# Performance work log

Measured on AMD Instinct MI355X. Metric: run time of the kernel, lower is better.

The kernel has to match this reference:

```python
import jax, jax.numpy as jnp
import numpy as np

B, C, T, H, W = 8, 512, 8, 28, 28
DI, DO = 256, 512  # dim_inner, dim_out
INIT_STD = 0.01
BN_EPS = 1e-5


def conv1x1(x, w, b):
    # 1x1x1 Conv3d == channel contraction. x: [B,C,T,H,W], w: [O,C], b: [O]
    return jnp.einsum('bcthw,oc->bothw', x, w) + b[None, :, None, None, None]


def setup_inputs() -> dict:
    key = jax.random.key(0)
    ks = jax.random.split(key, 8)
    x = jax.random.normal(ks[0], (B, C, T, H, W), jnp.float32)
    theta_w = INIT_STD * jax.random.normal(ks[1], (DI, C), jnp.float32)
    phi_w = INIT_STD * jax.random.normal(ks[2], (DI, C), jnp.float32)
    g_w = INIT_STD * jax.random.normal(ks[3], (DI, C), jnp.float32)
    out_w = INIT_STD * jax.random.normal(ks[4], (DO, DI), jnp.float32)
    theta_b = jnp.zeros((DI,), jnp.float32)
    phi_b = jnp.zeros((DI,), jnp.float32)
    g_b = jnp.zeros((DI,), jnp.float32)
    out_b = jnp.zeros((DO,), jnp.float32)
    bn_gamma = jnp.ones((DO,), jnp.float32)  # BN_INIT_GAMMA = 1.0
    bn_beta = jnp.zeros((DO,), jnp.float32)
    return {"x": x, "theta_w": theta_w, "theta_b": theta_b, "phi_w": phi_w,
            "phi_b": phi_b, "g_w": g_w, "g_b": g_b, "out_w": out_w,
            "out_b": out_b, "bn_gamma": bn_gamma, "bn_beta": bn_beta}


def reference(x, theta_w, theta_b, phi_w, phi_b, g_w, g_b, out_w, out_b, bn_gamma, bn_beta):
    b, c, t, h, w = x.shape
    scale = DI ** (-0.5)
    # theta on full resolution
    theta = conv1x1(x, theta_w, theta_b).reshape(b, DI, -1)          # [B,DI,N]
    # MaxPool3d((1,2,2)) with stride (1,2,2): H,W even -> block max
    mp = x.reshape(b, c, t, h // 2, 2, w // 2, 2).max(axis=(4, 6))   # [B,C,T,H/2,W/2]
    phi = conv1x1(mp, phi_w, phi_b).reshape(b, DI, -1)               # [B,DI,M]
    g = conv1x1(mp, g_w, g_b).reshape(b, DI, -1)                     # [B,DI,M]
    # attention: theta^T phi -> [B,N,M], scaled softmax over M
    logits = jnp.einsum('bdn,bdm->bnm', theta, phi) * scale
    p = jax.nn.softmax(logits, axis=-1)
    # t = g @ p^T -> [B,DI,N]
    tt = jnp.einsum('bdm,bnm->bdn', g, p).reshape(b, DI, t, h, w)
    out = conv1x1(tt, out_w, out_b)                                  # [B,DO,T,H,W]
    # BatchNorm3d (training-mode batch statistics over B,T,H,W)
    mean = out.mean(axis=(0, 2, 3, 4), keepdims=True)
    var = out.var(axis=(0, 2, 3, 4), keepdims=True)
    out = (out - mean) * jax.lax.rsqrt(var + BN_EPS)
    out = out * bn_gamma[None, :, None, None, None] + bn_beta[None, :, None, None, None]
    return out + x
```

## Files before the change

### kernel.cpp

```cpp
#include <hip/hip_runtime.h>
#include <hip/hip_bf16.h>

#define B_ 8
#define C_ 512
#define T_ 8
#define H_ 28
#define W_ 28
#define N_ (T_*H_*W_)
#define HP_ 14
#define WP_ 14
#define M_ (T_*HP_*WP_)
#define DI_ 256
#define DO_ 512
#define BN_EPS 1e-5f
#define SCALE_LOG2E 0.090168440055560214f
#define PSUM_COLS 392

typedef __attribute__((ext_vector_type(8))) short short8;
typedef __attribute__((ext_vector_type(4))) float float4v;
typedef __attribute__((ext_vector_type(2))) float float2v;

__device__ inline unsigned short f2bf(float f) {
    union { float f; unsigned int u; } v; v.f = f;
    unsigned int u = v.u;
    return (unsigned short)((u + 0x7FFFu + ((u >> 16) & 1u)) >> 16);
}
__device__ inline float bf2f(unsigned short h) {
    union { unsigned int u; float f; } v; v.u = ((unsigned int)h) << 16;
    return v.f;
}

__global__ void xpose_x(const float* __restrict__ x, unsigned short* __restrict__ xT) {
    __shared__ float tile[64][65];
    int b = blockIdx.z;
    int c0 = blockIdx.y * 64, n0 = blockIdx.x * 64;
    const float* src = x + (size_t)b * C_ * N_;
    int tx = threadIdx.x & 63, ty = threadIdx.x >> 6;
#pragma unroll
    for (int i = 0; i < 16; i++) {
        int c = ty + i * 4;
        tile[c][tx] = src[(size_t)(c0 + c) * N_ + n0 + tx];
    }
    __syncthreads();
    unsigned short* d = xT + ((size_t)b * N_ + n0) * C_ + c0;
#pragma unroll
    for (int i = 0; i < 16; i++) {
        int n = ty + i * 4;
        d[(size_t)n * C_ + tx] = f2bf(tile[tx][n]);
    }
}

__global__ void pool_xpose(const float* __restrict__ x, unsigned short* __restrict__ mpT) {
    __shared__ unsigned short tile[196][72];
    int b = blockIdx.z, t = blockIdx.y, c0 = blockIdx.x * 64;
    const float* src = x + (((size_t)b * C_ + c0) * T_ + t) * 784;
    for (int idx = threadIdx.x; idx < 64 * 196; idx += 256) {
        int cc = idx / 196, p = idx - cc * 196;
        int hp = p / 14, wp = p - hp * 14;
        const float* r0 = src + (size_t)cc * T_ * 784 + (2 * hp) * 28 + 2 * wp;
        float2v a = *(const float2v*)r0;
        float2v c = *(const float2v*)(r0 + 28);
        float m = fmaxf(fmaxf(a.x, a.y), fmaxf(c.x, c.y));
        tile[p][cc] = f2bf(m);
    }
    __syncthreads();
    unsigned short* d = mpT + ((size_t)b * M_ + t * 196) * C_ + c0;
    for (int idx = threadIdx.x; idx < 196 * 64; idx += 256) {
        int p = idx >> 6, cc = idx & 63;
        d[(size_t)p * C_ + cc] = tile[p][cc];
    }
}

__global__ void cast_w(const float* __restrict__ s, unsigned short* __restrict__ d, int n) {
    int i = blockIdx.x * 256 + threadIdx.x;
    if (i < n) d[i] = f2bf(s[i]);
}

template<int BIAS_MODE>
__global__ __launch_bounds__(256) void btgemm(
        const unsigned short* __restrict__ A, size_t strideAb,
        const unsigned short* __restrict__ Bm, size_t strideBb,
        unsigned short* __restrict__ Dp, size_t strideDb,
        const float* __restrict__ bias, int Mdim, int Ndim, int Kdim) {
    int b = blockIdx.z;
    const unsigned short* Ab = A + (size_t)b * strideAb;
    const unsigned short* Bb = Bm + (size_t)b * strideBb;
    int m0 = blockIdx.x * 64, n0 = blockIdx.y * 64;
    int wave = threadIdx.x >> 6, lane = threadIdx.x & 63;
    int wm = (wave >> 1) * 32, wn = (wave & 1) * 32;
    int lr = lane & 15, lk = lane >> 4;
    float4v acc[2][2] = {};
    for (int k0 = 0; k0 < Kdim; k0 += 32) {
        short8 a[2], bb[2];
#pragma unroll
        for (int i = 0; i < 2; i++) {
            int ar = m0 + wm + i * 16 + lr; if (ar >= Mdim) ar = Mdim - 1;
            a[i] = *(const short8*)(Ab + (size_t)ar * Kdim + k0 + lk * 8);
            int br = n0 + wn + i * 16 + lr; if (br >= Ndim) br = Ndim - 1;
            bb[i] = *(const short8*)(Bb + (size_t)br * Kdim + k0 + lk * 8);
        }
#pragma unroll
        for (int i = 0; i < 2; i++)
#pragma unroll
            for (int j = 0; j < 2; j++)
                acc[i][j] = __builtin_amdgcn_mfma_f32_16x16x32_bf16(a[i], bb[j], acc[i][j], 0, 0, 0);
    }
#pragma unroll
    for (int i = 0; i < 2; i++)
#pragma unroll
        for (int j = 0; j < 2; j++) {
            int col = n0 + wn + j * 16 + lr;
#pragma unroll
            for (int r = 0; r < 4; r++) {
                int row = m0 + wm + i * 16 + lk * 4 + r;
                if (row < Mdim && col < Ndim) {
                    float v = acc[i][j][r];
                    if (BIAS_MODE == 1) v += bias[col];
                    else if (BIAS_MODE == 2) v += bias[row];
                    Dp[(size_t)b * strideDb + (size_t)row * Ndim + col] = f2bf(v);
                }
            }
        }
}

__global__ __launch_bounds__(256, 2) void theta_gemm(
        const unsigned short* __restrict__ xT, const unsigned short* __restrict__ wq,
        unsigned short* __restrict__ thetaT, const float* __restrict__ bias) {
    __shared__ __align__(16) unsigned short wqs[2][32][512];
    const int bid = blockIdx.x;
    const int b = bid & 7;
    const int nblk = bid >> 3;
    const int wave = threadIdx.x >> 6, lane = threadIdx.x & 63;
    const int lr = lane & 15, lk = lane >> 4;
    const unsigned short* Ab = xT + ((size_t)b * N_ + nblk * 128 + wave * 32) * C_;

    short8 a[2][16];
#pragma unroll
    for (int i = 0; i < 2; i++)
#pragma unroll
        for (int kd = 0; kd < 16; kd++)
            a[i][kd] = *(const short8*)(Ab + (size_t)(i * 16 + lr) * C_ + kd * 32 + lk * 8);

    auto stage = [&](int bufi, int t) {
#pragma unroll
        for (int j = 0; j < 8; j++) {
            int row = wave * 8 + j;
            int qq = (lane * 16) ^ ((row & 7) << 4);
            const unsigned short* src = wq + (size_t)(t * 32 + row) * C_ + (qq >> 1);
            unsigned short* dst = &wqs[bufi][0][0] + row * 512;
            __builtin_amdgcn_global_load_lds(
                (const __attribute__((address_space(1))) unsigned int*)src,
                (__attribute__((address_space(3))) unsigned int*)dst, 16, 0, 0);
        }
    };

    stage(0, 0);
    const int hq = (lk * 16) ^ ((lr & 7) << 4);
    unsigned short* D = thetaT + ((size_t)b * N_ + nblk * 128 + wave * 32) * DI_;
    int buf = 0;
#pragma unroll
    for (int t = 0; t < 8; t++) {
        if (t < 7) {
            stage(buf ^ 1, t + 1);
            asm volatile("s_waitcnt vmcnt(8)" ::: "memory");
        } else {
            asm volatile("s_waitcnt vmcnt(0)" ::: "memory");
        }
        __syncthreads();
        const char* W = (const char*)&wqs[buf][0][0];
        float4v acc[2][2] = {};
#pragma unroll
        for (int kd = 0; kd < 16; kd++) {
            short8 b0 = *(const short8*)(W + lr * 1024 + ((kd * 64) ^ hq));
            short8 b1 = *(const short8*)(W + (16 + lr) * 1024 + ((kd * 64) ^ hq));
            acc[0][0] = __builtin_amdgcn_mfma_f32_16x16x32_bf16(a[0][kd], b0, acc[0][0], 0, 0, 0);
            acc[0][1] = __builtin_amdgcn_mfma_f32_16x16x32_bf16(a[0][kd], b1, acc[0][1], 0, 0, 0);
            acc[1][0] = __builtin_amdgcn_mfma_f32_16x16x32_bf16(a[1][kd], b0, acc[1][0], 0, 0, 0);
            acc[1][1] = __builtin_amdgcn_mfma_f32_16x16x32_bf16(a[1][kd], b1, acc[1][1], 0, 0, 0);
        }
#pragma unroll
        for (int i = 0; i < 2; i++)
#pragma unroll
            for (int j = 0; j < 2; j++) {
                int col = t * 32 + j * 16 + lr;
                float bv = bias[col];
#pragma unroll
                for (int r = 0; r < 4; r++) {
                    int row = i * 16 + lk * 4 + r;
                    D[(size_t)row * DI_ + col] = f2bf(acc[i][j][r] + bv);
                }
            }
        __syncthreads();
        buf ^= 1;
    }
}

__global__ __launch_bounds__(256, 2) void out_gemm(
        const unsigned short* __restrict__ wo,
        const unsigned short* __restrict__ Bh, const unsigned short* __restrict__ Bl,
        float* __restrict__ Dp, const float* __restrict__ bias,
        float* __restrict__ psum) {
    __shared__ __align__(16) unsigned short tts[2][2][32][256];
    const int bid = blockIdx.x;
    const int b = bid & 7;
    const int rem = bid >> 3;
    const int doblk = rem & 3;
    const int nchunk = rem >> 2;
    const int wave = threadIdx.x >> 6, lane = threadIdx.x & 63;
    const int lr = lane & 15, lk = lane >> 4;
    const unsigned short* Ab = wo + (size_t)(doblk * 128 + wave * 32) * DI_;
    const unsigned short* BhB = Bh + ((size_t)b * N_ + nchunk * 128) * DI_;
    const unsigned short* BlB = Bl + ((size_t)b * N_ + nchunk * 128) * DI_;

    short8 a[2][8];
#pragma unroll
    for (int i = 0; i < 2; i++)
#pragma unroll
        for (int kd = 0; kd < 8; kd++)
            a[i][kd] = *(const short8*)(Ab + (size_t)(i * 16 + lr) * DI_ + kd * 32 + lk * 8);

    auto stage = [&](int bufi, int t) {
#pragma unroll
        for (int p = 0; p < 2; p++) {
            const unsigned short* S = p ? BlB : BhB;
#pragma unroll
            for (int j = 0; j < 4; j++) {
                int chunk = wave * 4 + j;
                int row = chunk * 2 + (lane >> 5);
                int qq = (((lane & 31) * 16)) ^ ((row & 7) << 4);
                const unsigned short* src = S + (size_t)(t * 32 + row) * DI_ + (qq >> 1);
                unsigned short* dst = &tts[bufi][p][0][0] + chunk * 512;
                __builtin_amdgcn_global_load_lds(
                    (const __attribute__((address_space(1))) unsigned int*)src,
                    (__attribute__((address_space(3))) unsigned int*)dst, 16, 0, 0);
            }
        }
    };

    stage(0, 0);
    const int hq = (lk * 16) ^ ((lr & 7) << 4);
    float4v acc[4][2][2] = {};
    int buf = 0;
#pragma unroll
    for (int t = 0; t < 4; t++) {
        if (t < 3) {
            stage(buf ^ 1, t + 1);
            asm volatile("s_waitcnt vmcnt(8)" ::: "memory");
        } else {
            asm volatile("s_waitcnt vmcnt(0)" ::: "memory");
        }
        __syncthreads();
        const char* th = (const char*)&tts[buf][0][0][0];
        const char* tl = (const char*)&tts[buf][1][0][0];
#pragma unroll
        for (int kd = 0; kd < 8; kd++) {
            short8 bh0 = *(const short8*)(th + lr * 512 + ((kd * 64) ^ hq));
            short8 bh1 = *(const short8*)(th + (16 + lr) * 512 + ((kd * 64) ^ hq));
            short8 bl0 = *(const short8*)(tl + lr * 512 + ((kd * 64) ^ hq));
            short8 bl1 = *(const short8*)(tl + (16 + lr) * 512 + ((kd * 64) ^ hq));
            acc[t][0][0] = __builtin_amdgcn_mfma_f32_16x16x32_bf16(a[0][kd], bh0, acc[t][0][0], 0, 0, 0);
            acc[t][0][0] = __builtin_amdgcn_mfma_f32_16x16x32_bf16(a[0][kd], bl0, acc[t][0][0], 0, 0, 0);
            acc[t][0][1] = __builtin_amdgcn_mfma_f32_16x16x32_bf16(a[0][kd], bh1, acc[t][0][1], 0, 0, 0);
            acc[t][0][1] = __builtin_amdgcn_mfma_f32_16x16x32_bf16(a[0][kd], bl1, acc[t][0][1], 0, 0, 0);
            acc[t][1][0] = __builtin_amdgcn_mfma_f32_16x16x32_bf16(a[1][kd], bh0, acc[t][1][0], 0, 0, 0);
            acc[t][1][0] = __builtin_amdgcn_mfma_f32_16x16x32_bf16(a[1][kd], bl0, acc[t][1][0], 0, 0, 0);
            acc[t][1][1] = __builtin_amdgcn_mfma_f32_16x16x32_bf16(a[1][kd], bh1, acc[t][1][1], 0, 0, 0);
            acc[t][1][1] = __builtin_amdgcn_mfma_f32_16x16x32_bf16(a[1][kd], bl1, acc[t][1][1], 0, 0, 0);
        }
        __syncthreads();
        buf ^= 1;
    }
    float* Db = Dp + (size_t)b * DO_ * N_;
    float s1[2][4] = {}, s2[2][4] = {};
#pragma unroll
    for (int t = 0; t < 4; t++)
#pragma unroll
        for (int i = 0; i < 2; i++)
#pragma unroll
            for (int r = 0; r < 4; r++) {
                int dorow = doblk * 128 + wave * 32 + i * 16 + lk * 4 + r;
                float bv = bias[dorow];
                float v0 = acc[t][i][0][r] + bv;
                float v1 = acc[t][i][1][r] + bv;
                int ncol = nchunk * 128 + t * 32 + lr;
                Db[(size_t)dorow * N_ + ncol] = v0;
                Db[(size_t)dorow * N_ + ncol + 16] = v1;
                s1[i][r] += v0 + v1;
                s2[i][r] += v0 * v0 + v1 * v1;
            }
#pragma unroll
    for (int m = 1; m < 16; m <<= 1)
#pragma unroll
        for (int i = 0; i < 2; i++)
#pragma unroll
            for (int r = 0; r < 4; r++) {
                s1[i][r] += __shfl_xor(s1[i][r], m, 64);
                s2[i][r] += __shfl_xor(s2[i][r], m, 64);
            }
    if (lr == 0) {
        int pcol = b * 49 + nchunk;
#pragma unroll
        for (int i = 0; i < 2; i++)
#pragma unroll
            for (int r = 0; r < 4; r++) {
                int row = doblk * 128 + wave * 32 + i * 16 + lk * 4 + r;
                psum[(size_t)row * PSUM_COLS + pcol] = s1[i][r];
                psum[(size_t)(DO_ + row) * PSUM_COLS + pcol] = s2[i][r];
            }
    }
}

__global__ __launch_bounds__(256, 2) void attn_k(
        const unsigned short* __restrict__ thetaT,
        const unsigned short* __restrict__ phiT,
        const unsigned short* __restrict__ g,
        unsigned short* __restrict__ ttH,
        unsigned short* __restrict__ ttL) {
    __shared__ __align__(16) unsigned short phi_s[2][32][256];
    __shared__ __align__(16) unsigned short g_s[2][256][32];
    __shared__ __align__(16) unsigned short plds[4][32][32];
    const int bid = blockIdx.x;
    const int b = bid & 7;
    const int nblk = bid >> 3;
    const int wave = threadIdx.x >> 6, lane = threadIdx.x & 63;
    const int lr = lane & 15, lk = lane >> 4;
    const int n0 = nblk * 128 + wave * 32;
    const unsigned short* Q  = thetaT + ((size_t)b * N_ + n0) * DI_;
    const unsigned short* Pg = phiT + (size_t)b * M_ * DI_;
    const unsigned short* G  = g + (size_t)b * DI_ * M_;

    short8 q[2][8];
#pragma unroll
    for (int i = 0; i < 2; i++)
#pragma unroll
        for (int kd = 0; kd < 8; kd++)
            q[i][kd] = *(const short8*)(Q + (size_t)(i * 16 + lr) * DI_ + kd * 32 + lk * 8);

    float4v acc[2][16] = {};
    float rs[2][4] = {};

    auto stage = [&](int bufi, int t) {
        const unsigned short* phiRow = Pg + (size_t)t * 32 * DI_;
#pragma unroll
        for (int j = 0; j < 4; j++) {
            int chunk = wave * 4 + j;
            int row = chunk * 2 + (lane >> 5);
            int qq = ((lane & 31) * 16) ^ ((row & 7) << 4);
            const unsigned short* src = phiRow + (size_t)row * DI_ + (qq >> 1);
            unsigned short* dst = &phi_s[bufi][0][0] + chunk * 512;
            __builtin_amdgcn_global_load_lds(
                (const __attribute__((address_space(1))) unsigned int*)src,
                (__attribute__((address_space(3))) unsigned int*)dst, 16, 0, 0);
        }
#pragma unroll
        for (int j = 0; j < 4; j++) {
            int chunk = wave * 4 + j;
            int d = chunk * 16 + (lane >> 2);
            const unsigned short* src = G + (size_t)d * M_ + t * 32 + (lane & 3) * 8;
            unsigned short* dst = &g_s[bufi][0][0] + chunk * 512;
            __builtin_amdgcn_global_load_lds(
                (const __attribute__((address_space(1))) unsigned int*)src,
                (__attribute__((address_space(3))) unsigned int*)dst, 16, 0, 0);
        }
    };

    stage(0, 0);
    const int hq = (lk * 16) ^ ((lr & 7) << 4);
    int buf = 0;
    const int NT = M_ / 32;
    for (int t = 0; t < NT; t++) {
        if (t + 1 < NT) {
            stage(buf ^ 1, t + 1);
            asm volatile("s_waitcnt vmcnt(8)" ::: "memory");
        } else {
            asm volatile("s_waitcnt vmcnt(0)" ::: "memory");
        }
        __syncthreads();
        const char* phiB = (const char*)&phi_s[buf][0][0];
        float4v L[2][2] = {};
#pragma unroll
        for (int kd = 0; kd < 8; kd++) {
            short8 pb0 = *(const short8*)(phiB + lr * 512 + ((kd * 64) ^ hq));
            short8 pb1 = *(const short8*)(phiB + (16 + lr) * 512 + ((kd * 64) ^ hq));
            L[0][0] = __builtin_amdgcn_mfma_f32_16x16x32_bf16(q[0][kd], pb0, L[0][0], 0, 0, 0);
            L[0][1] = __builtin_amdgcn_mfma_f32_16x16x32_bf16(q[0][kd], pb1, L[0][1], 0, 0, 0);
            L[1][0] = __builtin_amdgcn_mfma_f32_16x16x32_bf16(q[1][kd], pb0, L[1][0], 0, 0, 0);
            L[1][1] = __builtin_amdgcn_mfma_f32_16x16x32_bf16(q[1][kd], pb1, L[1][1], 0, 0, 0);
        }
#pragma unroll
        for (int i = 0; i < 2; i++)
#pragma unroll
            for (int mj = 0; mj < 2; mj++)
#pragma unroll
                for (int r = 0; r < 4; r++) {
                    float e = exp2f(L[i][mj][r] * SCALE_LOG2E);
                    rs[i][r] += e;
                    plds[wave][i * 16 + lk * 4 + r][mj * 16 + lr] = f2bf(e);
                }
        short8 pa0 = *(const short8*)(&plds[wave][lr][lk * 8]);
        short8 pa1 = *(const short8*)(&plds[wave][16 + lr][lk * 8]);
#pragma unroll
        for (int fd = 0; fd < 16; fd++) {
            short8 gb = *(const short8*)(&g_s[buf][fd * 16 + lr][lk * 8]);
            acc[0][fd] = __builtin_amdgcn_mfma_f32_16x16x32_bf16(pa0, gb, acc[0][fd], 0, 0, 0);
            acc[1][fd] = __builtin_amdgcn_mfma_f32_16x16x32_bf16(pa1, gb, acc[1][fd], 0, 0, 0);
        }
        __syncthreads();
        buf ^= 1;
    }
#pragma unroll
    for (int s = 1; s < 16; s <<= 1)
#pragma unroll
        for (int i = 0; i < 2; i++)
#pragma unroll
            for (int r = 0; r < 4; r++) rs[i][r] += __shfl_xor(rs[i][r], s, 64);
    float inv[2][4];
#pragma unroll
    for (int i = 0; i < 2; i++)
#pragma unroll
        for (int r = 0; r < 4; r++) inv[i][r] = 1.0f / rs[i][r];
    unsigned short* OH = ttH + ((size_t)b * N_ + n0) * DI_;
    unsigned short* OL = ttL + ((size_t)b * N_ + n0) * DI_;
#pragma unroll
    for (int i = 0; i < 2; i++)
#pragma unroll
        for (int fd = 0; fd < 16; fd++)
#pragma unroll
            for (int r = 0; r < 4; r++) {
                float v = acc[i][fd][r] * inv[i][r];
                unsigned short h = f2bf(v);
                unsigned short l = f2bf(v - bf2f(h));
                size_t idx = (size_t)(i * 16 + lk * 4 + r) * DI_ + fd * 16 + lr;
                OH[idx] = h;
                OL[idx] = l;
            }
}

__global__ void bn_finalize(const float* __restrict__ psum, float* __restrict__ stats) {
    int o = blockIdx.x;
    float s = 0.f, q = 0.f;
    for (int c = threadIdx.x; c < PSUM_COLS; c += 256) {
        s += psum[(size_t)o * PSUM_COLS + c];
        q += psum[(size_t)(DO_ + o) * PSUM_COLS + c];
    }
#pragma unroll
    for (int m = 1; m < 64; m <<= 1) { s += __shfl_xor(s, m, 64); q += __shfl_xor(q, m, 64); }
    __shared__ float ws1[4], ws2[4];
    int wave = threadIdx.x >> 6;
    if ((threadIdx.x & 63) == 0) { ws1[wave] = s; ws2[wave] = q; }
    __syncthreads();
    if (threadIdx.x == 0) {
        double S = (double)ws1[0] + ws1[1] + ws1[2] + ws1[3];
        double Q = (double)ws2[0] + ws2[1] + ws2[2] + ws2[3];
        const double cnt = (double)(B_ * N_);
        double mean = S / cnt;
        double var = Q / cnt - mean * mean;
        stats[o] = (float)mean;
        stats[DO_ + o] = (float)(1.0 / sqrt(var + (double)BN_EPS));
    }
}

__global__ void bn_apply(float* __restrict__ out, const float* __restrict__ x,
                         const float* __restrict__ stats, const float* __restrict__ gamma,
                         const float* __restrict__ beta) {
    size_t i = (size_t)blockIdx.x * 256 + threadIdx.x;
    float4v v = ((const float4v*)out)[i];
    float4v xv = ((const float4v*)x)[i];
    int o = (int)((i * 4 / N_) % DO_);
    float mean = stats[o], rsig = stats[DO_ + o];
    float ga = gamma[o], be = beta[o];
    float4v r;
#pragma unroll
    for (int j = 0; j < 4; j++) r[j] = (v[j] - mean) * rsig * ga + be + xv[j];
    ((float4v*)out)[i] = r;
}

extern "C" void kernel_launch(void* const* d_in, const int* in_sizes, int n_in,
                              void* d_out, int out_size, void* d_ws, size_t ws_size,
                              hipStream_t stream) {
    const float* x       = (const float*)d_in[0];
    const float* theta_w = (const float*)d_in[1];
    const float* theta_b = (const float*)d_in[2];
    const float* phi_w   = (const float*)d_in[3];
    const float* phi_b   = (const float*)d_in[4];
    const float* g_w     = (const float*)d_in[5];
    const float* g_b     = (const float*)d_in[6];
    const float* out_w   = (const float*)d_in[7];
    const float* out_b   = (const float*)d_in[8];
    const float* bn_g    = (const float*)d_in[9];
    const float* bn_b    = (const float*)d_in[10];
    float* out = (float*)d_out;

    char* ws = (char*)d_ws;
    size_t off = 0;
    auto alloc = [&](size_t bytes) { void* p = ws + off; off += (bytes + 255) & ~(size_t)255; return p; };
    unsigned short* xT     = (unsigned short*)alloc((size_t)B_ * N_ * C_ * 2);
    unsigned short* mpT    = (unsigned short*)alloc((size_t)B_ * M_ * C_ * 2);
    unsigned short* thetaT = (unsigned short*)alloc((size_t)B_ * N_ * DI_ * 2);
    unsigned short* phiT   = (unsigned short*)alloc((size_t)B_ * M_ * DI_ * 2);
    unsigned short* gbuf   = (unsigned short*)alloc((size_t)B_ * DI_ * M_ * 2);
    unsigned short* wq     = (unsigned short*)alloc((size_t)DI_ * C_ * 2);
    unsigned short* wp     = (unsigned short*)alloc((size_t)DI_ * C_ * 2);
    unsigned short* wg     = (unsigned short*)alloc((size_t)DI_ * C_ * 2);
    unsigned short* wo     = (unsigned short*)alloc((size_t)DO_ * DI_ * 2);
    float* stats           = (float*)alloc((size_t)DO_ * 2 * 4);
    float* psum            = (float*)alloc((size_t)DO_ * 2 * PSUM_COLS * 4);
    unsigned short* ttH    = xT;
    unsigned short* ttL    = xT + (size_t)B_ * N_ * DI_;

    cast_w<<<(DI_ * C_ + 255) / 256, 256, 0, stream>>>(theta_w, wq, DI_ * C_);
    cast_w<<<(DI_ * C_ + 255) / 256, 256, 0, stream>>>(phi_w, wp, DI_ * C_);
    cast_w<<<(DI_ * C_ + 255) / 256, 256, 0, stream>>>(g_w, wg, DI_ * C_);
    cast_w<<<(DO_ * DI_ + 255) / 256, 256, 0, stream>>>(out_w, wo, DO_ * DI_);

    xpose_x<<<dim3(N_ / 64, C_ / 64, B_), 256, 0, stream>>>(x, xT);
    pool_xpose<<<dim3(C_ / 64, T_, B_), 256, 0, stream>>>(x, mpT);

    theta_gemm<<<392, 256, 0, stream>>>(xT, wq, thetaT, theta_b);
    btgemm<1><<<dim3((M_ + 63) / 64, DI_ / 64, B_), 256, 0, stream>>>(
        mpT, (size_t)M_ * C_, wp, 0, phiT, (size_t)M_ * DI_, phi_b, M_, DI_, C_);
    btgemm<2><<<dim3(DI_ / 64, (M_ + 63) / 64, B_), 256, 0, stream>>>(
        wg, 0, mpT, (size_t)M_ * C_, gbuf, (size_t)DI_ * M_, g_b, DI_, M_, C_);

    attn_k<<<dim3((N_ / 128) * 8), 256, 0, stream>>>(thetaT, phiT, gbuf, ttH, ttL);

    out_gemm<<<1568, 256, 0, stream>>>(wo, ttH, ttL, out, out_b, psum);

    bn_finalize<<<DO_, 256, 0, stream>>>(psum, stats);
    bn_apply<<<(size_t)B_ * DO_ * N_ / 4 / 256, 256, 0, stream>>>(out, x, stats, bn_g, bn_b);
}
```

Baseline: 383.4 us.

## Rewrite attention kernel with 32x32x16 MFMA and in-register P transpose

The attention kernel now uses 32x32x16 bf16 MFMAs, computing S transposed (phi as A, theta as B) so each lane holds a full column of probabilities. P is packed with v_cvt_pk_bf16_f32 and rearranged with v_permlane32_swap, which removes the per-wave LDS round trip for P and its reads. The g tile load gets an XOR swizzle to avoid LDS bank conflicts, s_setprio brackets the MFMA loops, and the row-sum reduction becomes a single cross-half shuffle. The risks are higher register pressure from the 8 float16 accumulators and correctness that depends on the exact lane layout of the swizzles and permlane swap.

```diff
diff --git a/kernel.cpp b/kernel.cpp
--- a/kernel.cpp
+++ b/kernel.cpp
@@ -18,6 +18,7 @@
 
 typedef __attribute__((ext_vector_type(8))) short short8;
 typedef __attribute__((ext_vector_type(4))) float float4v;
+typedef __attribute__((ext_vector_type(16))) float float16v;
 typedef __attribute__((ext_vector_type(2))) float float2v;
 
 __device__ inline unsigned short f2bf(float f) {
@@ -318,26 +319,23 @@
         unsigned short* __restrict__ ttL) {
     __shared__ __align__(16) unsigned short phi_s[2][32][256];
     __shared__ __align__(16) unsigned short g_s[2][256][32];
-    __shared__ __align__(16) unsigned short plds[4][32][32];
     const int bid = blockIdx.x;
     const int b = bid & 7;
     const int nblk = bid >> 3;
     const int wave = threadIdx.x >> 6, lane = threadIdx.x & 63;
-    const int lr = lane & 15, lk = lane >> 4;
+    const int l31 = lane & 31, hi = lane >> 5;
     const int n0 = nblk * 128 + wave * 32;
     const unsigned short* Q  = thetaT + ((size_t)b * N_ + n0) * DI_;
     const unsigned short* Pg = phiT + (size_t)b * M_ * DI_;
     const unsigned short* G  = g + (size_t)b * DI_ * M_;
 
-    short8 q[2][8];
-#pragma unroll
-    for (int i = 0; i < 2; i++)
-#pragma unroll
-        for (int kd = 0; kd < 8; kd++)
-            q[i][kd] = *(const short8*)(Q + (size_t)(i * 16 + lr) * DI_ + kd * 32 + lk * 8);
-
-    float4v acc[2][16] = {};
-    float rs[2][4] = {};
+    short8 q[16];
+#pragma unroll
+    for (int kb = 0; kb < 16; kb++)
+        q[kb] = *(const short8*)(Q + (size_t)l31 * DI_ + kb * 16 + hi * 8);
+
+    float16v acc[8] = {};
+    float rs = 0.f;
 
     auto stage = [&](int bufi, int t) {
         const unsigned short* phiRow = Pg + (size_t)t * 32 * DI_;
@@ -356,7 +354,8 @@
         for (int j = 0; j < 4; j++) {
             int chunk = wave * 4 + j;
             int d = chunk * 16 + (lane >> 2);
-            const unsigned short* src = G + (size_t)d * M_ + t * 32 + (lane & 3) * 8;
+            int mq = (lane & 3) ^ ((lane >> 3) & 3);
+            const unsigned short* src = G + (size_t)d * M_ + t * 32 + mq * 8;
             unsigned short* dst = &g_s[bufi][0][0] + chunk * 512;
             __builtin_amdgcn_global_load_lds(
                 (const __attribute__((address_space(1))) unsigned int*)src,
@@ -365,7 +364,8 @@
     };
 
     stage(0, 0);
-    const int hq = (lk * 16) ^ ((lr & 7) << 4);
+    const int pswz = (l31 & 7) << 4;
+    const int gswz = ((lane >> 1) & 3) << 4;
     int buf = 0;
     const int NT = M_ / 32;
     for (int t = 0; t < NT; t++) {
@@ -376,64 +376,75 @@
             asm volatile("s_waitcnt vmcnt(0)" ::: "memory");
         }
         __syncthreads();
+
         const char* phiB = (const char*)&phi_s[buf][0][0];
-        float4v L[2][2] = {};
-#pragma unroll
-        for (int kd = 0; kd < 8; kd++) {
-            short8 pb0 = *(const short8*)(phiB + lr * 512 + ((kd * 64) ^ hq));
-            short8 pb1 = *(const short8*)(phiB + (16 + lr) * 512 + ((kd * 64) ^ hq));
-            L[0][0] = __builtin_amdgcn_mfma_f32_16x16x32_bf16(q[0][kd], pb0, L[0][0], 0, 0, 0);
-            L[0][1] = __builtin_amdgcn_mfma_f32_16x16x32_bf16(q[0][kd], pb1, L[0][1], 0, 0, 0);
-            L[1][0] = __builtin_amdgcn_mfma_f32_16x16x32_bf16(q[1][kd], pb0, L[1][0], 0, 0, 0);
-            L[1][1] = __builtin_amdgcn_mfma_f32_16x16x32_bf16(q[1][kd], pb1, L[1][1], 0, 0, 0);
-        }
-#pragma unroll
-        for (int i = 0; i < 2; i++)
-#pragma unroll
-            for (int mj = 0; mj < 2; mj++)
-#pragma unroll
-                for (int r = 0; r < 4; r++) {
-                    float e = exp2f(L[i][mj][r] * SCALE_LOG2E);
-                    rs[i][r] += e;
-                    plds[wave][i * 16 + lk * 4 + r][mj * 16 + lr] = f2bf(e);
-                }
-        short8 pa0 = *(const short8*)(&plds[wave][lr][lk * 8]);
-        short8 pa1 = *(const short8*)(&plds[wave][16 + lr][lk * 8]);
-#pragma unroll
-        for (int fd = 0; fd < 16; fd++) {
-            short8 gb = *(const short8*)(&g_s[buf][fd * 16 + lr][lk * 8]);
-            acc[0][fd] = __builtin_amdgcn_mfma_f32_16x16x32_bf16(pa0, gb, acc[0][fd], 0, 0, 0);
-            acc[1][fd] = __builtin_amdgcn_mfma_f32_16x16x32_bf16(pa1, gb, acc[1][fd], 0, 0, 0);
-        }
+        float16v S = {};
+        __builtin_amdgcn_s_setprio(1);
+#pragma unroll
+        for (int kb = 0; kb < 16; kb++) {
+            short8 pha = *(const short8*)(phiB + l31 * 512 + ((kb * 32 + hi * 16) ^ pswz));
+            S = __builtin_amdgcn_mfma_f32_32x32x16_bf16(pha, q[kb], S, 0, 0, 0);
+        }
+        __builtin_amdgcn_s_setprio(0);
+
+        float p[16];
+#pragma unroll
+        for (int r = 0; r < 16; r++) {
+            p[r] = exp2f(S[r] * SCALE_LOG2E);
+            rs += p[r];
+        }
+        unsigned int pk0, pk1, pk2, pk3, pk4, pk5, pk6, pk7;
+        asm("v_cvt_pk_bf16_f32 %0, %1, %2" : "=v"(pk0) : "v"(p[0]),  "v"(p[1]));
+        asm("v_cvt_pk_bf16_f32 %0, %1, %2" : "=v"(pk1) : "v"(p[2]),  "v"(p[3]));
+        asm("v_cvt_pk_bf16_f32 %0, %1, %2" : "=v"(pk2) : "v"(p[4]),  "v"(p[5]));
+        asm("v_cvt_pk_bf16_f32 %0, %1, %2" : "=v"(pk3) : "v"(p[6]),  "v"(p[7]));
+        asm("v_cvt_pk_bf16_f32 %0, %1, %2" : "=v"(pk4) : "v"(p[8]),  "v"(p[9]));
+        asm("v_cvt_pk_bf16_f32 %0, %1, %2" : "=v"(pk5) : "v"(p[10]), "v"(p[11]));
+        asm("v_cvt_pk_bf16_f32 %0, %1, %2" : "=v"(pk6) : "v"(p[12]), "v"(p[13]));
+        asm("v_cvt_pk_bf16_f32 %0, %1, %2" : "=v"(pk7) : "v"(p[14]), "v"(p[15]));
+        asm("v_permlane32_swap_b32 %0, %1" : "+v"(pk0), "+v"(pk2));
+        asm("v_permlane32_swap_b32 %0, %1" : "+v"(pk1), "+v"(pk3));
+        asm("v_permlane32_swap_b32 %0, %1" : "+v"(pk4), "+v"(pk6));
+        asm("v_permlane32_swap_b32 %0, %1" : "+v"(pk5), "+v"(pk7));
+        union UF { unsigned int u[4]; short8 s; } pa0, pa1;
+        pa0.u[0] = pk0; pa0.u[1] = pk1; pa0.u[2] = pk2; pa0.u[3] = pk3;
+        pa1.u[0] = pk4; pa1.u[1] = pk5; pa1.u[2] = pk6; pa1.u[3] = pk7;
+
+        const char* gB = (const char*)&g_s[buf][0][0];
+        const int goff0 = (hi * 16) ^ gswz;
+        const int goff1 = (32 + hi * 16) ^ gswz;
+        __builtin_amdgcn_s_setprio(1);
+#pragma unroll
+        for (int dblk = 0; dblk < 8; dblk++) {
+            short8 gb0 = *(const short8*)(gB + (dblk * 32 + l31) * 64 + goff0);
+            short8 gb1 = *(const short8*)(gB + (dblk * 32 + l31) * 64 + goff1);
+            acc[dblk] = __builtin_amdgcn_mfma_f32_32x32x16_bf16(pa0.s, gb0, acc[dblk], 0, 0, 0);
+            acc[dblk] = __builtin_amdgcn_mfma_f32_32x32x16_bf16(pa1.s, gb1, acc[dblk], 0, 0, 0);
+        }
+        __builtin_amdgcn_s_setprio(0);
         __syncthreads();
         buf ^= 1;
     }
-#pragma unroll
-    for (int s = 1; s < 16; s <<= 1)
-#pragma unroll
-        for (int i = 0; i < 2; i++)
-#pragma unroll
-            for (int r = 0; r < 4; r++) rs[i][r] += __shfl_xor(rs[i][r], s, 64);
-    float inv[2][4];
-#pragma unroll
-    for (int i = 0; i < 2; i++)
-#pragma unroll
-        for (int r = 0; r < 4; r++) inv[i][r] = 1.0f / rs[i][r];
+
+    rs += __shfl_xor(rs, 32, 64);
+    float inv = 1.0f / rs;
+
     unsigned short* OH = ttH + ((size_t)b * N_ + n0) * DI_;
     unsigned short* OL = ttL + ((size_t)b * N_ + n0) * DI_;
 #pragma unroll
-    for (int i = 0; i < 2; i++)
-#pragma unroll
-        for (int fd = 0; fd < 16; fd++)
-#pragma unroll
-            for (int r = 0; r < 4; r++) {
-                float v = acc[i][fd][r] * inv[i][r];
-                unsigned short h = f2bf(v);
-                unsigned short l = f2bf(v - bf2f(h));
-                size_t idx = (size_t)(i * 16 + lk * 4 + r) * DI_ + fd * 16 + lr;
-                OH[idx] = h;
-                OL[idx] = l;
-            }
+    for (int reg = 0; reg < 16; reg++) {
+        int n_l = (reg & 3) + 8 * (reg >> 2) + 4 * hi;
+        float invn = __shfl(inv, n_l, 64);
+#pragma unroll
+        for (int dblk = 0; dblk < 8; dblk++) {
+            float v = acc[dblk][reg] * invn;
+            unsigned short h = f2bf(v);
+            unsigned short l = f2bf(v - bf2f(h));
+            size_t idx = (size_t)n_l * DI_ + dblk * 32 + l31;
+            OH[idx] = h;
+            OL[idx] = l;
+        }
+    }
 }
 
 __global__ void bn_finalize(const float* __restrict__ psum, float* __restrict__ stats) {
```

Result: no change. 383.7 us (+0.1%).
